# Kernel tuning notes

Hardware: AMD Instinct MI355X
Metric: run time of the kernel (lower is better)

Reference implementation:

```python
import jax, jax.numpy as jnp
import numpy as np

N = 50000
E = 1600000
IN_DIM = 32
EDGE_DIM = 32
HID = 64
OUT = 32


def setup_inputs() -> dict:
    key = jax.random.key(0)
    ks = jax.random.split(key, 12)
    x = jax.random.normal(ks[0], (N, IN_DIM), dtype=jnp.float32)
    edge_index = jax.random.randint(ks[1], (2, E), 0, N, dtype=jnp.int64)
    edge_attr = jax.random.normal(ks[2], (E, EDGE_DIM), dtype=jnp.float32)
    # MLP params: Linear(64->64), Linear(64->128), Linear(128->64), Linear(64->32)
    def lin(k, fan_in, fan_out):
        lim = 1.0 / np.sqrt(fan_in)
        kw, kb = jax.random.split(k)
        W = jax.random.uniform(kw, (fan_in, fan_out), minval=-lim, maxval=lim, dtype=jnp.float32)
        b = jax.random.uniform(kb, (fan_out,), minval=-lim, maxval=lim, dtype=jnp.float32)
        return W, b
    W1, b1 = lin(ks[3], IN_DIM + EDGE_DIM, HID)
    W2, b2 = lin(ks[4], HID, 2 * HID)
    W3, b3 = lin(ks[5], 2 * HID, HID)
    W4, b4 = lin(ks[6], HID, OUT)
    return {"x": x, "edge_index": edge_index, "edge_attr": edge_attr,
            "W1": W1, "b1": b1, "W2": W2, "b2": b2,
            "W3": W3, "b3": b3, "W4": W4, "b4": b4}


def reference(x, edge_index, edge_attr, W1, b1, W2, b2, W3, b3, W4, b4):
    # PyG MessagePassing (source_to_target): x_i = x[edge_index[1]] (target),
    # messages aggregated (mean) at target nodes edge_index[1].
    dst = edge_index[1]
    x_i = x[dst]                                   # [E, IN_DIM] gather
    m = jnp.concatenate([x_i, edge_attr], axis=-1)  # [E, 64]
    # 4-layer MLP with ReLU (dropout = identity at inference)
    m = jax.nn.relu(m @ W1 + b1)                   # [E, 64]
    m = jax.nn.relu(m @ W2 + b2)                   # [E, 128]
    m = jax.nn.relu(m @ W3 + b3)                   # [E, 64]
    m = jax.nn.relu(m @ W4 + b4)                   # [E, 32]
    # mean scatter to target nodes
    sums = jax.ops.segment_sum(m, dst, num_segments=N)          # [N, 32]
    cnt = jax.ops.segment_sum(jnp.ones((E,), m.dtype), dst, num_segments=N)
    out = sums / jnp.maximum(cnt, 1.0)[:, None]
    return out
```

## Files before the change

### kernel.cpp

```cpp
#include <hip/hip_runtime.h>
#include <hip/hip_bf16.h>

typedef __attribute__((ext_vector_type(8))) unsigned short u16x8;
typedef __attribute__((ext_vector_type(8))) __bf16 bf16x8;
typedef __attribute__((ext_vector_type(4))) float f32x4;

__device__ __forceinline__ unsigned pack_bf2(float lo, float hi) {
  unsigned a = __float_as_uint(lo) + 0x8000u;
  unsigned b = __float_as_uint(hi) + 0x8000u;
  return __builtin_amdgcn_perm(b, a, 0x07060302);
}

__device__ __forceinline__ unsigned short f2bf(float f) {
  unsigned u = __float_as_uint(f);
  return (unsigned short)((u + 0x7fffu + ((u >> 16) & 1u)) >> 16);
}

__device__ __forceinline__ int aswz(int row, int feat, int stride) {
  return row * stride + (((feat >> 3) ^ (row & 7)) << 4) + (feat & 7) * 2;
}

__global__ __launch_bounds__(256)
void prep_hist(const float* __restrict__ W1, const float* __restrict__ W2,
               const float* __restrict__ W3, const float* __restrict__ W4,
               unsigned short* __restrict__ wt,
               const int* __restrict__ ei, int* __restrict__ histI, int E, int N) {
  const int tid = threadIdx.x;
  const int i = blockIdx.x * 256 + tid;
  if (i < 22528) {
    float v; int n, k, K, base;
    if (i < 4096)       { n = i >> 6, k = i & 63;  K = 64;  base = 0;     v = W1[k * 64 + n]; }
    else if (i < 12288) { int j = i - 4096;  n = j >> 6, k = j & 63;  K = 64;  base = 4096;  v = W2[k * 128 + n]; }
    else if (i < 20480) { int j = i - 12288; n = j >> 7, k = j & 127; K = 128; base = 12288; v = W3[k * 64 + n]; }
    else                { int j = i - 20480; n = j >> 6, k = j & 63;  K = 64;  base = 20480; v = W4[k * 32 + n]; }
    int o = base + n * K + ((((k >> 3) ^ (n & 7)) << 3) + (k & 7));
    wt[o] = f2bf(v);
  }
  const int xcd = blockIdx.x & 7, kblk = blockIdx.x >> 3;
  const int nchunks = gridDim.x >> 3;
  const int chunk = (E + nchunks - 1) / nchunks;
  const int eBeg = kblk * chunk;
  const int eEnd = min(eBeg + chunk, E);
  const int dLo = (int)((long)xcd * N / 8);
  const int dHi = (int)((long)(xcd + 1) * N / 8);
  for (int e = eBeg + tid; e < eEnd; e += 256) {
    const int d = ei[E + e];
    if (d >= dLo && d < dHi) atomicAdd(&histI[d], 1);
  }
}

__global__ void scan_blocks(const int* __restrict__ histI, int* __restrict__ row_start,
                            int* __restrict__ blockSums, int N) {
  __shared__ int wsum[4];
  const int lane = threadIdx.x & 63, w = threadIdx.x >> 6;
  const int i0 = blockIdx.x * 2048 + threadIdx.x * 8;
  int v[8];
#pragma unroll
  for (int j = 0; j < 8; ++j) { int i = i0 + j; v[j] = (i < N) ? histI[i] : 0; }
  int s = 0;
#pragma unroll
  for (int j = 0; j < 8; ++j) { int t = v[j]; v[j] = s; s += t; }
  int ss = s;
#pragma unroll
  for (int d = 1; d < 64; d <<= 1) { int t = __shfl_up(ss, d, 64); if (lane >= d) ss += t; }
  if (lane == 63) wsum[w] = ss;
  __syncthreads();
  int wOff = 0;
#pragma unroll
  for (int k = 0; k < 4; ++k) if (k < w) wOff += wsum[k];
  const int tOff = wOff + (ss - s);
#pragma unroll
  for (int j = 0; j < 8; ++j) { int i = i0 + j; if (i < N) row_start[i] = tOff + v[j]; }
  if (threadIdx.x == 255) blockSums[blockIdx.x] = wOff + ss;
}

__global__ __launch_bounds__(256)
void fill_kernel(const int* __restrict__ ei, const int* __restrict__ row_start,
                 const int* __restrict__ blockSums, int* __restrict__ wcnt,
                 int2* __restrict__ edlist, float* __restrict__ out,
                 int E, int N, int nb) {
  __shared__ int spre[32];
  if (threadIdx.x == 0) {
    int acc = 0;
    for (int k = 0; k < nb; ++k) { spre[k] = acc; acc += blockSums[k]; }
  }
  __syncthreads();
  const int tid = threadIdx.x;
  const int Ntot4 = N * 8;
  for (int i = blockIdx.x * 256 + tid; i < Ntot4; i += gridDim.x * 256)
    ((float4*)out)[i] = make_float4(0.f, 0.f, 0.f, 0.f);

  const int xcd = blockIdx.x & 7, kblk = blockIdx.x >> 3;
  const int nchunks = gridDim.x >> 3;
  const int chunk = (E + nchunks - 1) / nchunks;
  const int eBeg = kblk * chunk;
  const int eEnd = min(eBeg + chunk, E);
  const int dLo = (int)((long)xcd * N / 8);
  const int dHi = (int)((long)(xcd + 1) * N / 8);
  for (int e = eBeg + tid; e < eEnd; e += 256) {
    const int d = ei[E + e];
    if (d >= dLo && d < dHi) {
      const int slot = atomicAdd(&wcnt[d], 1);
      edlist[row_start[d] + spre[d >> 11] + slot] = make_int2(e, d);
    }
  }
}

template <int MT, int KS, int SS, int DS>
__device__ __forceinline__ void mlp_layer(const unsigned char* src, unsigned char* dst,
                                          const unsigned char* wl, const float* biasL, int lane) {
  const int edge = lane & 15, g = lane >> 4;
  asm volatile("s_waitcnt lgkmcnt(0)" ::: "memory");
  u16x8 bfrag[KS];
#pragma unroll
  for (int ks = 0; ks < KS; ++ks)
    bfrag[ks] = *(const u16x8*)(src + aswz(edge, ks * 32 + g * 8, SS));
#pragma unroll
  for (int mt = 0; mt < MT; ++mt) {
    const int n = mt * 16 + edge;
    u16x8 af[KS];
#pragma unroll
    for (int ks = 0; ks < KS; ++ks)
      af[ks] = *(const u16x8*)(wl + n * (KS * 64) + (((ks * 4 + g) ^ (edge & 7)) << 4));
    const float4 bv = *(const float4*)(biasL + mt * 16 + g * 4);
    f32x4 acc = {bv.x, bv.y, bv.z, bv.w};
    __builtin_amdgcn_s_setprio(1);
#pragma unroll
    for (int ks = 0; ks < KS; ++ks)
      acc = __builtin_amdgcn_mfma_f32_16x16x32_bf16(
          __builtin_bit_cast(bf16x8, af[ks]), __builtin_bit_cast(bf16x8, bfrag[ks]),
          acc, 0, 0, 0);
    __builtin_amdgcn_s_setprio(0);
    const int fb = mt * 16 + g * 4;
    uint2 q;
    q.x = pack_bf2(fmaxf(acc[0], 0.f), fmaxf(acc[1], 0.f));
    q.y = pack_bf2(fmaxf(acc[2], 0.f), fmaxf(acc[3], 0.f));
    *(uint2*)(dst + aswz(edge, fb, DS)) = q;
  }
}

__device__ __forceinline__ void load_tile(int ebase, int E, const int2* __restrict__ edlist,
                                          const float* __restrict__ x, const float* __restrict__ ea,
                                          const int* __restrict__ histI,
                                          int lane, float4& xa, float4& xb, float4& ya, float4& yb,
                                          int& dstA, int& cntA) {
  const int el = ebase + (lane >> 2);
  const int part = lane & 3;
  xa = make_float4(0.f, 0.f, 0.f, 0.f); xb = xa; ya = xa; yb = xa;
  if (el < E) {
    const int2 ed = edlist[el];
    const float4* xp = (const float4*)(x + (size_t)ed.y * 32 + part * 8);
    xa = xp[0]; xb = xp[1];
    const float4* ep = (const float4*)(ea + (size_t)ed.x * 32 + part * 8);
    ya = ep[0]; yb = ep[1];
  }
  const int pos = ebase + (lane & 15);
  dstA = -1; cntA = 1;
  if (pos < E) {
    dstA = edlist[pos].y;
    cntA = histI[dstA];
  }
}

#define BIAS_OFF 45056
#define ACT_OFF  46208

__global__ __launch_bounds__(1024, 4)
void gnn_main(const float* __restrict__ x, const int2* __restrict__ edlist,
              const float* __restrict__ ea, const unsigned short* __restrict__ wt,
              const int* __restrict__ histI,
              const float* __restrict__ b1, const float* __restrict__ b2,
              const float* __restrict__ b3, const float* __restrict__ b4,
              float* __restrict__ out, int E, int numTiles) {
  __shared__ __align__(16) unsigned char lds[ACT_OFF + 16 * 6144];
  {
    const u16x8* gw = (const u16x8*)wt;
    u16x8* lw = (u16x8*)lds;
    for (int i = threadIdx.x; i < 2816; i += 1024) lw[i] = gw[i];
    float* biasW = (float*)(lds + BIAS_OFF);
    for (int i = threadIdx.x; i < 288; i += 1024) {
      float v;
      if (i < 64) v = b1[i];
      else if (i < 192) v = b2[i - 64];
      else if (i < 256) v = b3[i - 192];
      else v = b4[i - 256];
      biasW[i] = v;
    }
  }
  __syncthreads();

  const int lane = threadIdx.x & 63, wid = threadIdx.x >> 6;
  const int li = lane & 15, g = lane >> 4;
  const float* biasLds = (const float*)(lds + BIAS_OFF);
  unsigned char* buf0 = lds + ACT_OFF + wid * 6144;
  unsigned char* buf1 = buf0 + 4096;
  const unsigned char* wl1 = lds;
  const unsigned char* wl2 = lds + 8192;
  const unsigned char* wl3 = lds + 24576;
  const unsigned char* wl4 = lds + 40960;

  const int wgl = blockIdx.x * 16 + wid;
  const int wstride = gridDim.x * 16;

  float4 xa, xb, ya, yb; int dstA = -1, cntA = 1;
  if (wgl < numTiles) load_tile(wgl * 16, E, edlist, x, ea, histI, lane, xa, xb, ya, yb, dstA, cntA);

  for (int tile = wgl; tile < numTiles; tile += wstride) {
    uint4 hx, he;
    hx.x = pack_bf2(xa.x, xa.y); hx.y = pack_bf2(xa.z, xa.w);
    hx.z = pack_bf2(xb.x, xb.y); hx.w = pack_bf2(xb.z, xb.w);
    he.x = pack_bf2(ya.x, ya.y); he.y = pack_bf2(ya.z, ya.w);
    he.z = pack_bf2(yb.x, yb.y); he.w = pack_bf2(yb.z, yb.w);
    const int e2 = lane >> 2, part = lane & 3;
    *(uint4*)(buf0 + aswz(e2, part * 8, 256)) = hx;
    *(uint4*)(buf0 + aswz(e2, 32 + part * 8, 256)) = he;

    const int curDst = dstA, curCnt = cntA;

    const int nt = tile + wstride;
    float4 nxa, nxb, nya, nyb; int nd = -1, nc = 1;
    if (nt < numTiles) load_tile(nt * 16, E, edlist, x, ea, histI, lane, nxa, nxb, nya, nyb, nd, nc);
    else { nxa = make_float4(0,0,0,0); nxb = nxa; nya = nxa; nyb = nxa; }

    mlp_layer<4, 2, 256, 128>(buf0, buf1, wl1, biasLds + 0,   lane);
    mlp_layer<8, 2, 128, 256>(buf1, buf0, wl2, biasLds + 64,  lane);
    mlp_layer<4, 4, 256, 128>(buf0, buf1, wl3, biasLds + 192, lane);

    asm volatile("s_waitcnt lgkmcnt(0)" ::: "memory");
    u16x8 bf4[2];
#pragma unroll
    for (int ks = 0; ks < 2; ++ks)
      bf4[ks] = *(const u16x8*)(buf1 + aswz(li, ks * 32 + g * 8, 128));
    float vals[8];
#pragma unroll
    for (int mt = 0; mt < 2; ++mt) {
      const int n = mt * 16 + li;
      u16x8 af[2];
#pragma unroll
      for (int ks = 0; ks < 2; ++ks)
        af[ks] = *(const u16x8*)(wl4 + n * 128 + (((ks * 4 + g) ^ (li & 7)) << 4));
      const float4 bv = *(const float4*)(biasLds + 256 + mt * 16 + g * 4);
      f32x4 acc = {bv.x, bv.y, bv.z, bv.w};
      __builtin_amdgcn_s_setprio(1);
#pragma unroll
      for (int ks = 0; ks < 2; ++ks)
        acc = __builtin_amdgcn_mfma_f32_16x16x32_bf16(
            __builtin_bit_cast(bf16x8, af[ks]), __builtin_bit_cast(bf16x8, bf4[ks]),
            acc, 0, 0, 0);
      __builtin_amdgcn_s_setprio(0);
#pragma unroll
      for (int r = 0; r < 4; ++r) vals[mt * 4 + r] = fmaxf(acc[r], 0.f);
    }

    const int prev = __shfl_up(curDst, 1, 16);
    const bool is_head = (li == 0) || (prev != curDst);
    const unsigned long long hb = __ballot(is_head);
    const unsigned gm = (unsigned)((hb >> (g * 16)) & 0xFFFFu);
    const unsigned below = gm & ((1u << li) | ((1u << li) - 1u));
    const int dist = li - (31 - __clz(below));
#pragma unroll
    for (int d = 1; d < 16; d <<= 1) {
#pragma unroll
      for (int t = 0; t < 8; ++t) {
        const float tv = __shfl_up(vals[t], d, 16);
        if (dist >= d) vals[t] += tv;
      }
    }
    const bool is_end = (li == 15) || ((gm >> (li + 1)) & 1u);
    if (is_end && curDst >= 0) {
      const float inv = 1.0f / (float)curCnt;
      float* op = out + (size_t)curDst * 32 + g * 4;
#pragma unroll
      for (int t = 0; t < 4; ++t) unsafeAtomicAdd(op + t, vals[t] * inv);
#pragma unroll
      for (int t = 0; t < 4; ++t) unsafeAtomicAdd(op + 16 + t, vals[4 + t] * inv);
    }

    xa = nxa; xb = nxb; ya = nya; yb = nyb; dstA = nd; cntA = nc;
  }
}

extern "C" void kernel_launch(void* const* d_in, const int* in_sizes, int n_in,
                              void* d_out, int out_size, void* d_ws, size_t ws_size,
                              hipStream_t stream) {
  const float* x  = (const float*)d_in[0];
  const int*   ei = (const int*)d_in[1];
  const float* ea = (const float*)d_in[2];
  const float* W1 = (const float*)d_in[3];
  const float* b1 = (const float*)d_in[4];
  const float* W2 = (const float*)d_in[5];
  const float* b2 = (const float*)d_in[6];
  const float* W3 = (const float*)d_in[7];
  const float* b3 = (const float*)d_in[8];
  const float* W4 = (const float*)d_in[9];
  const float* b4 = (const float*)d_in[10];
  const int N = in_sizes[0] / 32;
  const int E = in_sizes[1] / 2;
  float* out = (float*)d_out;

  char* ws = (char*)d_ws;
  size_t off = 0;
  auto alloc = [&](size_t bytes) { size_t o = off; off += (bytes + 255) & ~(size_t)255; return o; };
  size_t hist_off = alloc((size_t)N * 4);
  size_t wcnt_off = alloc((size_t)N * 4);
  int* histI      = (int*)(ws + hist_off);
  int* wcnt       = (int*)(ws + wcnt_off);
  int* row_start  = (int*)(ws + alloc((size_t)(N + 1) * 4));
  int* blockSums  = (int*)(ws + alloc(256 * 4));
  int2* edlist    = (int2*)(ws + alloc((size_t)E * 8));
  unsigned short* wt = (unsigned short*)(ws + alloc(22528 * 2));

  hipMemsetAsync(ws + hist_off, 0, (wcnt_off - hist_off) + (size_t)N * 4, stream);

  prep_hist<<<2048, 256, 0, stream>>>(W1, W2, W3, W4, wt, ei, histI, E, N);
  const int nb = (N + 2047) / 2048;
  scan_blocks<<<nb, 256, 0, stream>>>(histI, row_start, blockSums, N);
  fill_kernel<<<2048, 256, 0, stream>>>(ei, row_start, blockSums, wcnt, edlist, out, E, N, nb);
  const int numTiles = (E + 15) / 16;
  gnn_main<<<256, 1024, 0, stream>>>(x, edlist, ea, wt, histI,
                                     b1, b2, b3, b4, out, E, numTiles);
}
```

Before: 314.5 us.

## Vectorize index reads, fold slot counter into row_start, keep layer-2 weights in registers

The histogram and fill passes now read destination indices as int4, four per thread, with chunks rounded to multiples of four. The fill pass increments row_start atomically instead of a separate wcnt array, which removes one buffer, one read and part of the memset. The main kernel loads layer-2 weight fragments into registers once per wave instead of re-reading them from LDS on every tile. Holding those weights in registers adds 64 VGPRs per thread at 1024 threads per block, which risks spills or lower occupancy.

```diff
diff --git a/kernel.cpp b/kernel.cpp
--- a/kernel.cpp
+++ b/kernel.cpp
@@ -38,12 +38,20 @@
   }
   const int xcd = blockIdx.x & 7, kblk = blockIdx.x >> 3;
   const int nchunks = gridDim.x >> 3;
-  const int chunk = (E + nchunks - 1) / nchunks;
+  const int chunk = (((E + nchunks - 1) / nchunks) + 3) & ~3;
   const int eBeg = kblk * chunk;
   const int eEnd = min(eBeg + chunk, E);
   const int dLo = (int)((long)xcd * N / 8);
   const int dHi = (int)((long)(xcd + 1) * N / 8);
-  for (int e = eBeg + tid; e < eEnd; e += 256) {
+  int e0 = eBeg + tid * 4;
+  for (; e0 + 3 < eEnd; e0 += 1024) {
+    const int4 d4 = *(const int4*)(ei + E + e0);
+    if (d4.x >= dLo && d4.x < dHi) atomicAdd(&histI[d4.x], 1);
+    if (d4.y >= dLo && d4.y < dHi) atomicAdd(&histI[d4.y], 1);
+    if (d4.z >= dLo && d4.z < dHi) atomicAdd(&histI[d4.z], 1);
+    if (d4.w >= dLo && d4.w < dHi) atomicAdd(&histI[d4.w], 1);
+  }
+  for (int e = e0; e < eEnd; ++e) {
     const int d = ei[E + e];
     if (d >= dLo && d < dHi) atomicAdd(&histI[d], 1);
   }
@@ -75,10 +83,9 @@
 }
 
 __global__ __launch_bounds__(256)
-void fill_kernel(const int* __restrict__ ei, const int* __restrict__ row_start,
-                 const int* __restrict__ blockSums, int* __restrict__ wcnt,
-                 int2* __restrict__ edlist, float* __restrict__ out,
-                 int E, int N, int nb) {
+void fill_kernel(const int* __restrict__ ei, int* __restrict__ row_start,
+                 const int* __restrict__ blockSums, int2* __restrict__ edlist,
+                 float* __restrict__ out, int E, int N, int nb) {
   __shared__ int spre[32];
   if (threadIdx.x == 0) {
     int acc = 0;
@@ -92,16 +99,29 @@
 
   const int xcd = blockIdx.x & 7, kblk = blockIdx.x >> 3;
   const int nchunks = gridDim.x >> 3;
-  const int chunk = (E + nchunks - 1) / nchunks;
+  const int chunk = (((E + nchunks - 1) / nchunks) + 3) & ~3;
   const int eBeg = kblk * chunk;
   const int eEnd = min(eBeg + chunk, E);
   const int dLo = (int)((long)xcd * N / 8);
   const int dHi = (int)((long)(xcd + 1) * N / 8);
-  for (int e = eBeg + tid; e < eEnd; e += 256) {
+  int e0 = eBeg + tid * 4;
+  for (; e0 + 3 < eEnd; e0 += 1024) {
+    const int4 d4 = *(const int4*)(ei + E + e0);
+    const int dv[4] = {d4.x, d4.y, d4.z, d4.w};
+#pragma unroll
+    for (int j = 0; j < 4; ++j) {
+      const int d = dv[j];
+      if (d >= dLo && d < dHi) {
+        const int pos = atomicAdd(&row_start[d], 1) + spre[d >> 11];
+        edlist[pos] = make_int2(e0 + j, d);
+      }
+    }
+  }
+  for (int e = e0; e < eEnd; ++e) {
     const int d = ei[E + e];
     if (d >= dLo && d < dHi) {
-      const int slot = atomicAdd(&wcnt[d], 1);
-      edlist[row_start[d] + spre[d >> 11] + slot] = make_int2(e, d);
+      const int pos = atomicAdd(&row_start[d], 1) + spre[d >> 11];
+      edlist[pos] = make_int2(e, d);
     }
   }
 }
@@ -129,6 +149,35 @@
     for (int ks = 0; ks < KS; ++ks)
       acc = __builtin_amdgcn_mfma_f32_16x16x32_bf16(
           __builtin_bit_cast(bf16x8, af[ks]), __builtin_bit_cast(bf16x8, bfrag[ks]),
+          acc, 0, 0, 0);
+    __builtin_amdgcn_s_setprio(0);
+    const int fb = mt * 16 + g * 4;
+    uint2 q;
+    q.x = pack_bf2(fmaxf(acc[0], 0.f), fmaxf(acc[1], 0.f));
+    q.y = pack_bf2(fmaxf(acc[2], 0.f), fmaxf(acc[3], 0.f));
+    *(uint2*)(dst + aswz(edge, fb, DS)) = q;
+  }
+}
+
+template <int MT, int KS, int SS, int DS>
+__device__ __forceinline__ void mlp_layerR(const unsigned char* src, unsigned char* dst,
+                                           const u16x8 (&wf)[MT][KS],
+                                           const float* biasL, int lane) {
+  const int edge = lane & 15, g = lane >> 4;
+  asm volatile("s_waitcnt lgkmcnt(0)" ::: "memory");
+  u16x8 bfrag[KS];
+#pragma unroll
+  for (int ks = 0; ks < KS; ++ks)
+    bfrag[ks] = *(const u16x8*)(src + aswz(edge, ks * 32 + g * 8, SS));
+#pragma unroll
+  for (int mt = 0; mt < MT; ++mt) {
+    const float4 bv = *(const float4*)(biasL + mt * 16 + g * 4);
+    f32x4 acc = {bv.x, bv.y, bv.z, bv.w};
+    __builtin_amdgcn_s_setprio(1);
+#pragma unroll
+    for (int ks = 0; ks < KS; ++ks)
+      acc = __builtin_amdgcn_mfma_f32_16x16x32_bf16(
+          __builtin_bit_cast(bf16x8, wf[mt][ks]), __builtin_bit_cast(bf16x8, bfrag[ks]),
           acc, 0, 0, 0);
     __builtin_amdgcn_s_setprio(0);
     const int fb = mt * 16 + g * 4;
@@ -199,6 +248,13 @@
   const unsigned char* wl3 = lds + 24576;
   const unsigned char* wl4 = lds + 40960;
 
+  u16x8 wf2[8][2];
+#pragma unroll
+  for (int mt = 0; mt < 8; ++mt)
+#pragma unroll
+    for (int ks = 0; ks < 2; ++ks)
+      wf2[mt][ks] = *(const u16x8*)(wl2 + (mt * 16 + li) * 128 + (((ks * 4 + g) ^ (li & 7)) << 4));
+
   const int wgl = blockIdx.x * 16 + wid;
   const int wstride = gridDim.x * 16;
 
@@ -223,7 +279,7 @@
     else { nxa = make_float4(0,0,0,0); nxb = nxa; nya = nxa; nyb = nxa; }
 
     mlp_layer<4, 2, 256, 128>(buf0, buf1, wl1, biasLds + 0,   lane);
-    mlp_layer<8, 2, 128, 256>(buf1, buf0, wl2, biasLds + 64,  lane);
+    mlp_layerR<8, 2, 128, 256>(buf1, buf0, wf2, biasLds + 64, lane);
     mlp_layer<4, 4, 256, 128>(buf0, buf1, wl3, biasLds + 192, lane);
 
     asm volatile("s_waitcnt lgkmcnt(0)" ::: "memory");
@@ -302,20 +358,18 @@
   size_t off = 0;
   auto alloc = [&](size_t bytes) { size_t o = off; off += (bytes + 255) & ~(size_t)255; return o; };
   size_t hist_off = alloc((size_t)N * 4);
-  size_t wcnt_off = alloc((size_t)N * 4);
   int* histI      = (int*)(ws + hist_off);
-  int* wcnt       = (int*)(ws + wcnt_off);
   int* row_start  = (int*)(ws + alloc((size_t)(N + 1) * 4));
   int* blockSums  = (int*)(ws + alloc(256 * 4));
   int2* edlist    = (int2*)(ws + alloc((size_t)E * 8));
   unsigned short* wt = (unsigned short*)(ws + alloc(22528 * 2));
 
-  hipMemsetAsync(ws + hist_off, 0, (wcnt_off - hist_off) + (size_t)N * 4, stream);
+  hipMemsetAsync(histI, 0, (size_t)N * 4, stream);
 
   prep_hist<<<2048, 256, 0, stream>>>(W1, W2, W3, W4, wt, ei, histI, E, N);
   const int nb = (N + 2047) / 2048;
   scan_blocks<<<nb, 256, 0, stream>>>(histI, row_start, blockSums, N);
-  fill_kernel<<<2048, 256, 0, stream>>>(ei, row_start, blockSums, wcnt, edlist, out, E, N, nb);
+  fill_kernel<<<2048, 256, 0, stream>>>(ei, row_start, blockSums, edlist, out, E, N, nb);
   const int numTiles = (E + 15) / 16;
   gnn_main<<<256, 1024, 0, stream>>>(x, edlist, ea, wt, histI,
                                      b1, b2, b3, b4, out, E, numTiles);
```

Result: slower. 419.0 us (+33.2%).
